# Optimization experiments

Measured on AMD Instinct MI355X. Metric: run time of the kernel, lower is better.

## Reference

```python
import jax, jax.numpy as jnp
from jax import lax
import numpy as np

N = 16384          # number of input points
C_IN = 64          # in_channels
C_OUT = 128        # out_channels
RATIO = 0.25
K = 16
N_CLUSTERS = int(N * RATIO)   # 4096
BN_EPS = 1e-5


def setup_inputs() -> dict:
    key = jax.random.key(0)
    k1, k2, k3 = jax.random.split(key, 3)
    x = jax.random.normal(k1, (N, C_IN), jnp.float32)
    pos = jax.random.normal(k2, (N, 3), jnp.float32)
    batch = jnp.zeros((N,), jnp.int32)  # single point cloud
    fan_in = 3 + C_IN
    W = jax.random.normal(k3, (C_OUT, fan_in), jnp.float32) / np.sqrt(fan_in)  # Linear(67->128, bias=False)
    gamma = jnp.ones((C_OUT,), jnp.float32)   # BatchNorm1d weight
    beta = jnp.zeros((C_OUT,), jnp.float32)   # BatchNorm1d bias
    return {"x": x, "pos": pos, "batch": batch, "W": W, "gamma": gamma, "beta": beta}


def fps(pos, n_samples):
    """Farthest point sampling, deterministic start at index 0."""
    n = pos.shape[0]

    def step(carry, _):
        min_d, last = carry
        d = jnp.sum((pos - pos[last]) ** 2, axis=-1)       # [N]
        min_d = jnp.minimum(min_d, d)
        nxt = jnp.argmax(min_d).astype(jnp.int32)
        return (min_d, nxt), nxt

    init = (jnp.full((n,), jnp.inf, pos.dtype), jnp.int32(0))
    _, rest = lax.scan(step, init, None, length=n_samples - 1)
    return jnp.concatenate([jnp.zeros((1,), jnp.int32), rest])


def knn(pos, batch, clusters, k):
    """For each cluster center, k nearest points (batch-masked). Returns [M, k] indices into pos."""
    qpos = pos[clusters]                                    # [M, 3]
    # squared distances via expansion to avoid [M, N, 3] intermediate
    d = (jnp.sum(qpos * qpos, axis=1)[:, None]
         + jnp.sum(pos * pos, axis=1)[None, :]
         - 2.0 * (qpos @ pos.T))                            # [M, N]
    same = batch[clusters][:, None] == batch[None, :]
    d = jnp.where(same, d, jnp.inf)
    _, nbr = lax.top_k(-d, k)                               # [M, k]
    return nbr.astype(jnp.int32)


def reference(x, pos, batch, W, gamma, beta):
    id_clusters = fps(pos, N_CLUSTERS)                      # [M]
    sub_batch = batch[id_clusters]
    nbr = knn(pos, batch, id_clusters, K)                   # [M, K] indices into pos

    # flatten to edge list (row 0 = query id in [0, M), row 1 = neighbor id in [0, N))
    q_flat = jnp.repeat(jnp.arange(N_CLUSTERS, dtype=jnp.int32), K)  # [M*K]
    n_flat = nbr.reshape(-1)                                         # [M*K]

    # NOTE: faithful to source: query indices index the FULL pos array
    relative_pos = pos[n_flat] - pos[q_flat]                # [M*K, 3]
    grouped = jnp.concatenate([relative_pos, x[n_flat]], axis=1)  # [M*K, 3+C_IN]

    # MLP = Linear(no bias) + BatchNorm1d (training stats) + ReLU
    h = grouped @ W.T                                       # [M*K, C_OUT]
    mean = jnp.mean(h, axis=0)
    var = jnp.mean((h - mean) ** 2, axis=0)                 # biased var, as torch BN
    h = gamma * (h - mean) * lax.rsqrt(var + BN_EPS) + beta
    h = jax.nn.relu(h)

    out = jax.ops.segment_max(h, q_flat, num_segments=N_CLUSTERS)  # scatter_max
    sub_pos = pos[id_clusters]
    return out, sub_pos, sub_batch
```

## Files before the change

kernel.cpp:

```cpp
#include <hip/hip_runtime.h>
#include <math.h>

#define N_PTS 16384
#define N_CLUSTERS 4096
#define KNN_K 16
#define C_IN 64
#define C_OUT 128
#define FAN_IN 67
#define N_ROWS (N_CLUSTERS * KNN_K)
#define NBINS 256

typedef float vf2 __attribute__((ext_vector_type(2)));
typedef unsigned long long u64;
typedef u64 u64x2 __attribute__((ext_vector_type(2)));

__global__ void init_kernel(const float* __restrict__ pos, float* __restrict__ pp,
                            float* __restrict__ cz) {
#pragma clang fp contract(off)
    int i = blockIdx.x * 256 + threadIdx.x;
    if (i < N_PTS) {
        float a = pos[i * 3 + 0], b = pos[i * 3 + 1], c = pos[i * 3 + 2];
        pp[i] = ((a * a) + (b * b)) + (c * c);
    }
    if (blockIdx.x == 0 && threadIdx.x < 256) cz[threadIdx.x] = 0.0f;
}

__global__ __launch_bounds__(512)
__attribute__((amdgpu_waves_per_eu(2, 2)))
void fps_kernel(const float* __restrict__ pos, int* __restrict__ clusters) {
#pragma clang fp contract(off)
    __shared__ unsigned short s_perm[N_PTS];
    __shared__ int s_cluster[N_CLUSTERS];
    __shared__ int s_hist[NBINS];
    __shared__ float s_red[16];
    __shared__ __align__(16) u64 s_wkey[2][8];
    const int t = threadIdx.x;
    const int w = t >> 6, lane = t & 63;
    const int wbase = w << 11;

    float txmin = __builtin_inff(), txmax = -__builtin_inff();
#pragma unroll
    for (int k = 0; k < 32; ++k) {
        const float xv = pos[(t + (k << 9)) * 3];
        txmin = fminf(txmin, xv);
        txmax = fmaxf(txmax, xv);
    }
#pragma unroll
    for (int off = 32; off >= 1; off >>= 1) {
        txmin = fminf(txmin, __shfl_xor(txmin, off));
        txmax = fmaxf(txmax, __shfl_xor(txmax, off));
    }
    if (lane == 0) { s_red[w] = txmin; s_red[8 + w] = txmax; }
    if (t < NBINS) s_hist[t] = 0;
    if (t == 0) s_cluster[0] = 0;
    __syncthreads();
    float gxmin = s_red[0], gxmax = s_red[8];
#pragma unroll
    for (int i = 1; i < 8; ++i) {
        gxmin = fminf(gxmin, s_red[i]);
        gxmax = fmaxf(gxmax, s_red[8 + i]);
    }
    const float binv = (float)NBINS / (gxmax - gxmin);

#pragma unroll
    for (int k = 0; k < 32; ++k) {
        const int i = t + (k << 9);
        int b = (int)((pos[i * 3] - gxmin) * binv);
        b = (b < 0) ? 0 : ((b > NBINS - 1) ? NBINS - 1 : b);
        atomicAdd(&s_hist[b], 1);
    }
    __syncthreads();
    if (t == 0) {
        int run = 0;
        for (int b = 0; b < NBINS; ++b) {
            const int c = s_hist[b];
            s_hist[b] = run;
            run += c;
        }
    }
    __syncthreads();
#pragma unroll
    for (int k = 0; k < 32; ++k) {
        const int i = t + (k << 9);
        int b = (int)((pos[i * 3] - gxmin) * binv);
        b = (b < 0) ? 0 : ((b > NBINS - 1) ? NBINS - 1 : b);
        const int dest = atomicAdd(&s_hist[b], 1);
        s_perm[dest] = (unsigned short)i;
    }
    __syncthreads();

    vf2 ax[16], ay[16], az[16], mdv[16];
    unsigned int oid[16];
    float mnx = __builtin_inff(), mxx = -__builtin_inff();
#pragma unroll
    for (int a = 0; a < 16; ++a) {
        const int s0 = wbase + (((a << 1) | 0) << 6) + lane;
        const int s1 = wbase + (((a << 1) | 1) << 6) + lane;
        const unsigned int o0 = s_perm[s0], o1 = s_perm[s1];
        oid[a] = (o1 << 16) | o0;
        ax[a] = (vf2){pos[o0 * 3 + 0], pos[o1 * 3 + 0]};
        ay[a] = (vf2){pos[o0 * 3 + 1], pos[o1 * 3 + 1]};
        az[a] = (vf2){pos[o0 * 3 + 2], pos[o1 * 3 + 2]};
        mdv[a] = (vf2){__builtin_inff(), __builtin_inff()};
        mnx = fminf(mnx, fminf(ax[a].x, ax[a].y));
        mxx = fmaxf(mxx, fmaxf(ax[a].x, ax[a].y));
    }
#pragma unroll
    for (int off = 32; off >= 1; off >>= 1) {
        mnx = fminf(mnx, __shfl_xor(mnx, off));
        mxx = fmaxf(mxx, __shfl_xor(mxx, off));
    }
    if (lane == 0) { s_red[w] = mnx; s_red[8 + w] = mxx; }
    __syncthreads();
    const float lo = s_red[w], hi = s_red[8 + w];

    float lx = pos[0], ly = pos[1], lz = pos[2];
    u64 wkey = 0;

#define PAIR_STAGE(CTRL, RM)                                                          \
    do {                                                                              \
        unsigned int ohi = (unsigned int)__builtin_amdgcn_update_dpp(                 \
            0, (int)hi_, (CTRL), (RM), 0xF, false);                                   \
        unsigned int olo = (unsigned int)__builtin_amdgcn_update_dpp(                 \
            0, (int)lo_, (CTRL), (RM), 0xF, false);                                   \
        u64 cur = ((u64)hi_ << 32) | lo_;                                             \
        u64 oth = ((u64)ohi << 32) | olo;                                             \
        if (oth > cur) { hi_ = ohi; lo_ = olo; }                                      \
    } while (0)

#define UPDATE_AND_KEY()                                                              \
    do {                                                                              \
        const vf2 lxv = (vf2){lx, lx}, lyv = (vf2){ly, ly}, lzv = (vf2){lz, lz};      \
        vf2 bm = (vf2){0.0f, 0.0f};                                                   \
        _Pragma("unroll")                                                             \
        for (int a = 0; a < 16; ++a) {                                                \
            vf2 dx = ax[a] - lxv;                                                     \
            vf2 dy = ay[a] - lyv;                                                     \
            vf2 dz = az[a] - lzv;                                                     \
            vf2 d = ((dx * dx) + (dy * dy)) + (dz * dz);                              \
            vf2 m;                                                                    \
            m.x = fminf(mdv[a].x, d.x);                                               \
            m.y = fminf(mdv[a].y, d.y);                                               \
            mdv[a] = m;                                                               \
            bm = __builtin_elementwise_max(bm, m);                                    \
        }                                                                             \
        const float bv = fmaxf(bm.x, bm.y);                                           \
        unsigned int mi = 0xffffffffu;                                                \
        _Pragma("unroll")                                                             \
        for (int a = 0; a < 16; ++a) {                                                \
            const unsigned int c0 =                                                   \
                (mdv[a].x == bv) ? (oid[a] & 0xffffu) : 0xffffffffu;                  \
            const unsigned int c1 =                                                   \
                (mdv[a].y == bv) ? (oid[a] >> 16) : 0xffffffffu;                      \
            const unsigned int cc = (c0 < c1) ? c0 : c1;                              \
            mi = (cc < mi) ? cc : mi;                                                 \
        }                                                                             \
        unsigned int hi_ = __float_as_uint(bv);                                       \
        unsigned int lo_ = ~mi;                                                       \
        PAIR_STAGE(0x111, 0xF);                                                       \
        PAIR_STAGE(0x112, 0xF);                                                       \
        PAIR_STAGE(0x114, 0xF);                                                       \
        PAIR_STAGE(0x118, 0xF);                                                       \
        PAIR_STAGE(0x142, 0xA);                                                       \
        PAIR_STAGE(0x143, 0xC);                                                       \
        wkey = ((u64)hi_ << 32) | lo_;                                                \
    } while (0)

    UPDATE_AND_KEY();
    if (lane == 63) s_wkey[1][w] = wkey;
    __syncthreads();

    for (int step = 1; step < N_CLUSTERS; ++step) {
        const int p = step & 1;
        const u64x2* kp = (const u64x2*)&s_wkey[p][0];
        const u64x2 k0 = kp[0], k1 = kp[1], k2 = kp[2], k3 = kp[3];
        u64 b0 = (k0.x > k0.y) ? k0.x : k0.y;
        u64 b1 = (k1.x > k1.y) ? k1.x : k1.y;
        u64 b2 = (k2.x > k2.y) ? k2.x : k2.y;
        u64 b3 = (k3.x > k3.y) ? k3.x : k3.y;
        b0 = (b1 > b0) ? b1 : b0;
        b2 = (b3 > b2) ? b3 : b2;
        const u64 bkey = (b2 > b0) ? b2 : b0;
        const unsigned int win = ~((unsigned int)bkey);
        if (t == 0) s_cluster[step] = (int)win;

        const unsigned int winu =
            (unsigned int)__builtin_amdgcn_readfirstlane((int)win);
        lx = pos[winu * 3 + 0];
        ly = pos[winu * 3 + 1];
        lz = pos[winu * 3 + 2];

        const u64 own = s_wkey[p][w];
        const float wm = __uint_as_float((unsigned int)(own >> 32));
        const float dm = fmaxf(fmaxf(lo - lx, lx - hi), 0.0f);
        const bool act = (dm * dm < wm);
        if (__builtin_amdgcn_readfirstlane((int)act)) UPDATE_AND_KEY();

        if (lane == 63) s_wkey[p ^ 1][w] = wkey;
        __syncthreads();
    }
#undef UPDATE_AND_KEY
#undef PAIR_STAGE

    for (int i = t; i < N_CLUSTERS; i += 512) clusters[i] = s_cluster[i];
}

__global__ __launch_bounds__(256) void knn_kernel(const float* __restrict__ pos,
                                                  const float* __restrict__ pp,
                                                  const int* __restrict__ clusters,
                                                  int* __restrict__ nbr) {
#pragma clang fp contract(off)
    __shared__ float s_d[8192];
    __shared__ float s_rv[4];
    __shared__ int   s_ri[4];
    __shared__ float s_tv[32];
    __shared__ int   s_ti[32];
    const int m = blockIdx.x, t = threadIdx.x;
    const int lane = t & 63, w = t >> 6;

    const int qi = clusters[m];
    const float qx = pos[qi * 3 + 0], qy = pos[qi * 3 + 1], qz = pos[qi * 3 + 2];
    const float qq = ((qx * qx) + (qy * qy)) + (qz * qz);

    for (int chunk = 0; chunk < 2; ++chunk) {
        const int base = chunk << 13;
        __syncthreads();
        for (int i = t; i < 8192; i += 256) {
            const int p = base + i;
            float dot = fmaf(qx, pos[p * 3 + 0], 0.0f);
            dot = fmaf(qy, pos[p * 3 + 1], dot);
            dot = fmaf(qz, pos[p * 3 + 2], dot);
            s_d[i] = (qq + pp[p]) - 2.0f * dot;
        }
        __syncthreads();
        for (int r = 0; r < KNN_K; ++r) {
            float bv = __builtin_inff();
            int   bi = 0x7fffffff;
            for (int i = t; i < 8192; i += 256) {
                float v = s_d[i];
                if (v < bv) { bv = v; bi = i; }
            }
#pragma unroll
            for (int off = 32; off >= 1; off >>= 1) {
                float ov = __shfl_down(bv, off);
                int   oi = __shfl_down(bi, off);
                if (ov < bv || (ov == bv && oi < bi)) { bv = ov; bi = oi; }
            }
            if (lane == 0) { s_rv[w] = bv; s_ri[w] = bi; }
            __syncthreads();
            if (t == 0) {
                float fv = s_rv[0]; int fi = s_ri[0];
#pragma unroll
                for (int ww = 1; ww < 4; ++ww) {
                    if (s_rv[ww] < fv || (s_rv[ww] == fv && s_ri[ww] < fi)) {
                        fv = s_rv[ww]; fi = s_ri[ww];
                    }
                }
                s_tv[chunk * 16 + r] = fv;
                s_ti[chunk * 16 + r] = base + fi;
                s_d[fi] = __builtin_inff();
            }
            __syncthreads();
        }
    }
    if (t == 0) {
        int a = 0, b = 0;
        for (int r = 0; r < KNN_K; ++r) {
            bool takeA;
            if (b >= 16) takeA = true;
            else if (a >= 16) takeA = false;
            else {
                float va = s_tv[a], vb = s_tv[16 + b];
                takeA = (va < vb) || (va == vb && s_ti[a] < s_ti[16 + b]);
            }
            nbr[m * KNN_K + r] = takeA ? s_ti[a] : s_ti[16 + b];
            if (takeA) ++a; else ++b;
        }
    }
}

template <int PASS>
__global__ __launch_bounds__(256) void mlp_kernel(const float* __restrict__ x,
                                                  const float* __restrict__ pos,
                                                  const int* __restrict__ nbr,
                                                  const float* __restrict__ W,
                                                  float* __restrict__ colsum,
                                                  float* __restrict__ colsumsq,
                                                  const float* __restrict__ ss,
                                                  const int* __restrict__ clusters,
                                                  const int* __restrict__ batch,
                                                  float* __restrict__ out) {
    __shared__ __align__(16) float At[FAN_IN][68];
    __shared__ __align__(16) float Wl[FAN_IN * 132];
    __shared__ float red0[128], red1[128];
    __shared__ float hm[8][132];
    const int tid = threadIdx.x;
    const int R0 = blockIdx.x * 64;

    for (int idx = tid; idx < FAN_IN * 128; idx += 256) {
        int i = idx >> 7, c = idx & 127;
        Wl[i * 132 + c] = W[c * FAN_IN + i];
    }
    {
        const int wv = tid >> 6, lane = tid & 63;
        for (int r = wv; r < 64; r += 4) {
            const int R = R0 + r;
            const int n = nbr[R];
            At[3 + lane][r] = x[n * C_IN + lane];
            if (lane < 3) {
                const int q = R >> 4;
                At[lane][r] = pos[n * 3 + lane] - pos[q * 3 + lane];
            }
        }
    }
    if (PASS == 1 && tid < 128) { red0[tid] = 0.0f; red1[tid] = 0.0f; }
    __syncthreads();

    const int g = tid & 31, rg = tid >> 5;
    const int c0 = g * 4, r0 = rg * 8;
    float acc[8][4];
#pragma unroll
    for (int a = 0; a < 8; ++a)
#pragma unroll
        for (int b = 0; b < 4; ++b) acc[a][b] = 0.0f;

    for (int i = 0; i < FAN_IN; ++i) {
        const float4 w4 = *(const float4*)&Wl[i * 132 + c0];
        const float4 a0 = *(const float4*)&At[i][r0];
        const float4 a1 = *(const float4*)&At[i][r0 + 4];
        const float av[8] = {a0.x, a0.y, a0.z, a0.w, a1.x, a1.y, a1.z, a1.w};
        const float wv4[4] = {w4.x, w4.y, w4.z, w4.w};
#pragma unroll
        for (int a = 0; a < 8; ++a)
#pragma unroll
            for (int b = 0; b < 4; ++b) acc[a][b] = fmaf(av[a], wv4[b], acc[a][b]);
    }

    if (PASS == 1) {
#pragma unroll
        for (int b = 0; b < 4; ++b) {
            float s = 0.0f, sq = 0.0f;
#pragma unroll
            for (int a = 0; a < 8; ++a) {
                s += acc[a][b];
                sq = fmaf(acc[a][b], acc[a][b], sq);
            }
            atomicAdd(&red0[c0 + b], s);
            atomicAdd(&red1[c0 + b], sq);
        }
        __syncthreads();
        if (tid < 128) {
            atomicAdd(&colsum[tid], red0[tid]);
            atomicAdd(&colsumsq[tid], red1[tid]);
        }
    } else {
#pragma unroll
        for (int b = 0; b < 4; ++b) {
            const float sc = ss[c0 + b], sh = ss[128 + c0 + b];
            float mx = -__builtin_inff();
#pragma unroll
            for (int a = 0; a < 8; ++a) mx = fmaxf(mx, fmaf(sc, acc[a][b], sh));
            hm[rg][c0 + b] = mx;
        }
        __syncthreads();
        for (int o = tid; o < 512; o += 256) {
            const int cl = o >> 7, c = o & 127;
            const float v = fmaxf(hm[2 * cl][c], hm[2 * cl + 1][c]);
            const int M = blockIdx.x * 4 + cl;
            out[M * 128 + c] = fmaxf(v, 0.0f);
        }
        if (tid < 12) {
            const int cl = tid / 3, l = tid % 3;
            const int M = blockIdx.x * 4 + cl;
            out[524288 + M * 3 + l] = pos[clusters[M] * 3 + l];
        } else if (tid < 16) {
            const int M = blockIdx.x * 4 + (tid - 12);
            out[536576 + M] = (float)batch[clusters[M]];
        }
    }
}

__global__ void stats_kernel(const float* __restrict__ colsum,
                             const float* __restrict__ colsumsq,
                             const float* __restrict__ gamma,
                             const float* __restrict__ beta,
                             float* __restrict__ ss) {
    const int c = threadIdx.x;
    const float inv_n = 1.0f / (float)N_ROWS;
    const float mean = colsum[c] * inv_n;
    float var = colsumsq[c] * inv_n - mean * mean;
    var = fmaxf(var, 0.0f);
    const float inv = rsqrtf(var + 1e-5f);
    const float sc = gamma[c] * inv;
    ss[c] = sc;
    ss[128 + c] = beta[c] - mean * sc;
}

extern "C" void kernel_launch(void* const* d_in, const int* in_sizes, int n_in,
                              void* d_out, int out_size, void* d_ws, size_t ws_size,
                              hipStream_t stream) {
    const float* x     = (const float*)d_in[0];
    const float* pos   = (const float*)d_in[1];
    const int*   batch = (const int*)d_in[2];
    const float* W     = (const float*)d_in[3];
    const float* gamma = (const float*)d_in[4];
    const float* beta  = (const float*)d_in[5];
    float* out = (float*)d_out;
    float* wsf = (float*)d_ws;

    int*   clusters = (int*)d_ws;
    int*   nbr      = clusters + 4096;
    float* pp       = wsf + 69632;
    float* colsum   = wsf + 86016;
    float* colsumsq = wsf + 86144;
    float* ss       = wsf + 86272;

    init_kernel<<<dim3(64), dim3(256), 0, stream>>>(pos, pp, colsum);
    fps_kernel<<<dim3(1), dim3(512), 0, stream>>>(pos, clusters);
    knn_kernel<<<dim3(N_CLUSTERS), dim3(256), 0, stream>>>(pos, pp, clusters, nbr);
    mlp_kernel<1><<<dim3(1024), dim3(256), 0, stream>>>(x, pos, nbr, W, colsum, colsumsq,
                                                        ss, clusters, batch, out);
    stats_kernel<<<dim3(1), dim3(128), 0, stream>>>(colsum, colsumsq, gamma, beta, ss);
    mlp_kernel<2><<<dim3(1024), dim3(256), 0, stream>>>(x, pos, nbr, W, colsum, colsumsq,
                                                        ss, clusters, batch, out);
}
```

Baseline: 5.036 ms.

## Partition FPS points into octants and prune waves with 3D bounding boxes

After: 5.991 ms. 19.0% more time.

```diff
diff --git a/kernel.cpp b/kernel.cpp
--- a/kernel.cpp
+++ b/kernel.cpp
@@ -8,7 +8,6 @@
 #define C_OUT 128
 #define FAN_IN 67
 #define N_ROWS (N_CLUSTERS * KNN_K)
-#define NBINS 256
 
 typedef float vf2 __attribute__((ext_vector_type(2)));
 typedef unsigned long long u64;
@@ -31,48 +30,54 @@
 #pragma clang fp contract(off)
     __shared__ unsigned short s_perm[N_PTS];
     __shared__ int s_cluster[N_CLUSTERS];
-    __shared__ int s_hist[NBINS];
-    __shared__ float s_red[16];
+    __shared__ int s_hist[8];
+    __shared__ float s_red[24];
     __shared__ __align__(16) u64 s_wkey[2][8];
     const int t = threadIdx.x;
     const int w = t >> 6, lane = t & 63;
     const int wbase = w << 11;
 
-    float txmin = __builtin_inff(), txmax = -__builtin_inff();
-#pragma unroll
-    for (int k = 0; k < 32; ++k) {
-        const float xv = pos[(t + (k << 9)) * 3];
-        txmin = fminf(txmin, xv);
-        txmax = fmaxf(txmax, xv);
-    }
-#pragma unroll
-    for (int off = 32; off >= 1; off >>= 1) {
-        txmin = fminf(txmin, __shfl_xor(txmin, off));
-        txmax = fmaxf(txmax, __shfl_xor(txmax, off));
-    }
-    if (lane == 0) { s_red[w] = txmin; s_red[8 + w] = txmax; }
-    if (t < NBINS) s_hist[t] = 0;
-    if (t == 0) s_cluster[0] = 0;
-    __syncthreads();
-    float gxmin = s_red[0], gxmax = s_red[8];
-#pragma unroll
-    for (int i = 1; i < 8; ++i) {
-        gxmin = fminf(gxmin, s_red[i]);
-        gxmax = fmaxf(gxmax, s_red[8 + i]);
-    }
-    const float binv = (float)NBINS / (gxmax - gxmin);
-
+    float sx = 0.0f, sy = 0.0f, sz = 0.0f;
 #pragma unroll
     for (int k = 0; k < 32; ++k) {
         const int i = t + (k << 9);
-        int b = (int)((pos[i * 3] - gxmin) * binv);
-        b = (b < 0) ? 0 : ((b > NBINS - 1) ? NBINS - 1 : b);
-        atomicAdd(&s_hist[b], 1);
+        sx += pos[i * 3 + 0];
+        sy += pos[i * 3 + 1];
+        sz += pos[i * 3 + 2];
+    }
+#pragma unroll
+    for (int off = 32; off >= 1; off >>= 1) {
+        sx += __shfl_xor(sx, off);
+        sy += __shfl_xor(sy, off);
+        sz += __shfl_xor(sz, off);
+    }
+    if (lane == 0) { s_red[w] = sx; s_red[8 + w] = sy; s_red[16 + w] = sz; }
+    if (t < 8) s_hist[t] = 0;
+    if (t == 0) s_cluster[0] = 0;
+    __syncthreads();
+    float tx = 0.0f, ty = 0.0f, tz = 0.0f;
+#pragma unroll
+    for (int i = 0; i < 8; ++i) {
+        tx += s_red[i];
+        ty += s_red[8 + i];
+        tz += s_red[16 + i];
+    }
+    const float mx = tx * (1.0f / N_PTS);
+    const float my = ty * (1.0f / N_PTS);
+    const float mz = tz * (1.0f / N_PTS);
+
+#pragma unroll
+    for (int k = 0; k < 32; ++k) {
+        const int i = t + (k << 9);
+        const int c = ((pos[i * 3 + 0] > mx) ? 4 : 0) |
+                      ((pos[i * 3 + 1] > my) ? 2 : 0) |
+                      ((pos[i * 3 + 2] > mz) ? 1 : 0);
+        atomicAdd(&s_hist[c], 1);
     }
     __syncthreads();
     if (t == 0) {
         int run = 0;
-        for (int b = 0; b < NBINS; ++b) {
+        for (int b = 0; b < 8; ++b) {
             const int c = s_hist[b];
             s_hist[b] = run;
             run += c;
@@ -82,16 +87,19 @@
 #pragma unroll
     for (int k = 0; k < 32; ++k) {
         const int i = t + (k << 9);
-        int b = (int)((pos[i * 3] - gxmin) * binv);
-        b = (b < 0) ? 0 : ((b > NBINS - 1) ? NBINS - 1 : b);
-        const int dest = atomicAdd(&s_hist[b], 1);
+        const int c = ((pos[i * 3 + 0] > mx) ? 4 : 0) |
+                      ((pos[i * 3 + 1] > my) ? 2 : 0) |
+                      ((pos[i * 3 + 2] > mz) ? 1 : 0);
+        const int dest = atomicAdd(&s_hist[c], 1);
         s_perm[dest] = (unsigned short)i;
     }
     __syncthreads();
 
     vf2 ax[16], ay[16], az[16], mdv[16];
     unsigned int oid[16];
-    float mnx = __builtin_inff(), mxx = -__builtin_inff();
+    float lox = __builtin_inff(), hix = -__builtin_inff();
+    float loy = __builtin_inff(), hiy = -__builtin_inff();
+    float loz = __builtin_inff(), hiz = -__builtin_inff();
 #pragma unroll
     for (int a = 0; a < 16; ++a) {
         const int s0 = wbase + (((a << 1) | 0) << 6) + lane;
@@ -102,17 +110,22 @@
         ay[a] = (vf2){pos[o0 * 3 + 1], pos[o1 * 3 + 1]};
         az[a] = (vf2){pos[o0 * 3 + 2], pos[o1 * 3 + 2]};
         mdv[a] = (vf2){__builtin_inff(), __builtin_inff()};
-        mnx = fminf(mnx, fminf(ax[a].x, ax[a].y));
-        mxx = fmaxf(mxx, fmaxf(ax[a].x, ax[a].y));
+        lox = fminf(lox, fminf(ax[a].x, ax[a].y));
+        hix = fmaxf(hix, fmaxf(ax[a].x, ax[a].y));
+        loy = fminf(loy, fminf(ay[a].x, ay[a].y));
+        hiy = fmaxf(hiy, fmaxf(ay[a].x, ay[a].y));
+        loz = fminf(loz, fminf(az[a].x, az[a].y));
+        hiz = fmaxf(hiz, fmaxf(az[a].x, az[a].y));
     }
 #pragma unroll
     for (int off = 32; off >= 1; off >>= 1) {
-        mnx = fminf(mnx, __shfl_xor(mnx, off));
-        mxx = fmaxf(mxx, __shfl_xor(mxx, off));
-    }
-    if (lane == 0) { s_red[w] = mnx; s_red[8 + w] = mxx; }
-    __syncthreads();
-    const float lo = s_red[w], hi = s_red[8 + w];
+        lox = fminf(lox, __shfl_xor(lox, off));
+        hix = fmaxf(hix, __shfl_xor(hix, off));
+        loy = fminf(loy, __shfl_xor(loy, off));
+        hiy = fmaxf(hiy, __shfl_xor(hiy, off));
+        loz = fminf(loz, __shfl_xor(loz, off));
+        hiz = fmaxf(hiz, __shfl_xor(hiz, off));
+    }
 
     float lx = pos[0], ly = pos[1], lz = pos[2];
     u64 wkey = 0;
@@ -192,8 +205,11 @@
 
         const u64 own = s_wkey[p][w];
         const float wm = __uint_as_float((unsigned int)(own >> 32));
-        const float dm = fmaxf(fmaxf(lo - lx, lx - hi), 0.0f);
-        const bool act = (dm * dm < wm);
+        const float dmx = fmaxf(fmaxf(lox - lx, lx - hix), 0.0f);
+        const float dmy = fmaxf(fmaxf(loy - ly, ly - hiy), 0.0f);
+        const float dmz = fmaxf(fmaxf(loz - lz, lz - hiz), 0.0f);
+        const float bnd = ((dmx * dmx) + (dmy * dmy)) + (dmz * dmz);
+        const bool act = (bnd < wm);
         if (__builtin_amdgcn_readfirstlane((int)act)) UPDATE_AND_KEY();
 
         if (lane == 63) s_wkey[p ^ 1][w] = wkey;
```
